# Optimization experiments

Measured on AMD Instinct MI355X. Metric: run time of the kernel, lower is better.

## Reference

```python
import jax, jax.numpy as jnp
import numpy as np

B, N, D, H = 4, 2048, 1024, 16
DH = D // H  # 64
EPS = 1e-5


def setup_inputs() -> dict:
    key = jax.random.key(0)
    k1, k2, k3, k4 = jax.random.split(key, 4)
    return {
        "x": jax.random.normal(k1, (B, N, D), dtype=jnp.float32),
        "g_ln": jnp.ones((D,), dtype=jnp.float32),
        "Wq": jax.random.normal(k2, (D, D), dtype=jnp.float32) * 0.02,
        "Wkv": jax.random.normal(k3, (D, 2 * D), dtype=jnp.float32) * 0.02,
        "Wo": jax.random.normal(k4, (D, D), dtype=jnp.float32) * 0.02,
    }


def reference(x, g_ln, Wq, Wkv, Wo):
    # LayerNorm (gamma only, no bias), as in repo-style LayerNorm
    mu = jnp.mean(x, axis=-1, keepdims=True)
    var = jnp.mean(jnp.square(x - mu), axis=-1, keepdims=True)
    xn = (x - mu) * jax.lax.rsqrt(var + EPS) * g_ln

    b, n, d = xn.shape
    q = (xn @ Wq).reshape(b, n, H, DH).transpose(0, 2, 1, 3)  # b h n d
    kv = xn @ Wkv
    k, v = jnp.split(kv, 2, axis=-1)
    k = k.reshape(b, n, H, DH).transpose(0, 2, 1, 3)
    v = v.reshape(b, n, H, DH).transpose(0, 2, 1, 3)

    scale = DH ** -0.5
    dots = jnp.einsum('bhid,bhjd->bhij', q, k) * scale

    # causal mask: mask out j > i
    mask_value = -jnp.finfo(dots.dtype).max
    causal = jnp.triu(jnp.ones((n, n), dtype=bool), k=1)
    dots = jnp.where(causal, mask_value, dots)

    # softmax in float32 (attn_fn = partial(F.softmax, dtype=torch.float32))
    attn = jax.nn.softmax(dots.astype(jnp.float32), axis=-1).astype(dots.dtype)

    out = jnp.einsum('bhij,bhjd->bhid', attn, v)
    out = out.transpose(0, 2, 1, 3).reshape(b, n, d)  # b n (h d)
    return out @ Wo
```

## Files before the change

kernel.cpp:

```cpp
#include <hip/hip_runtime.h>

typedef __bf16 bf16x8 __attribute__((ext_vector_type(8)));
typedef float  f32x4  __attribute__((ext_vector_type(4)));
typedef unsigned short u16;

typedef __attribute__((address_space(3))) unsigned lds_u32;
typedef __attribute__((address_space(1))) unsigned glob_u32;

__device__ __forceinline__ void gll16(const void* g, void* l) {
  __builtin_amdgcn_global_load_lds(
      (const glob_u32*)(unsigned long long)g,
      (lds_u32*)(unsigned)(unsigned long long)l, 16, 0, 0);
}

__device__ __forceinline__ u16 cvt_bf16(float f) {
  union { float f; unsigned u; } c; c.f = f;
  unsigned u = c.u;
  return (u16)((u + 0x7FFFu + ((u >> 16) & 1u)) >> 16);
}

__global__ void __launch_bounds__(256) transpose_cvt(const float* __restrict__ W,
                                                     u16* __restrict__ WT,
                                                     int K, int N) {
  __shared__ float t[32][33];
  int n0 = blockIdx.x * 32, k0 = blockIdx.y * 32;
  int tx = threadIdx.x, ty = threadIdx.y;
#pragma unroll
  for (int i = 0; i < 4; i++)
    t[ty + i * 8][tx] = W[(size_t)(k0 + ty + i * 8) * N + n0 + tx];
  __syncthreads();
#pragma unroll
  for (int i = 0; i < 4; i++)
    WT[(size_t)(n0 + ty + i * 8) * K + k0 + tx] = cvt_bf16(t[tx][ty + i * 8]);
}

__global__ void __launch_bounds__(256) ln_kernel(const float* __restrict__ x,
                                                 const float* __restrict__ g,
                                                 u16* __restrict__ xn) {
  int row = blockIdx.x, tid = threadIdx.x;
  const float4* xr = (const float4*)(x + (size_t)row * 1024);
  float4 v = xr[tid];
  float s  = v.x + v.y + v.z + v.w;
  float ss = v.x * v.x + v.y * v.y + v.z * v.z + v.w * v.w;
#pragma unroll
  for (int off = 32; off > 0; off >>= 1) {
    s  += __shfl_down(s, off);
    ss += __shfl_down(ss, off);
  }
  __shared__ float red[8];
  if ((tid & 63) == 0) { red[(tid >> 6) * 2] = s; red[(tid >> 6) * 2 + 1] = ss; }
  __syncthreads();
  s  = red[0] + red[2] + red[4] + red[6];
  ss = red[1] + red[3] + red[5] + red[7];
  float mean = s * (1.0f / 1024.0f);
  float var  = ss * (1.0f / 1024.0f) - mean * mean;
  float inv  = rsqrtf(var + 1e-5f);
  float4 gv = ((const float4*)g)[tid];
  unsigned p0 = (unsigned)cvt_bf16((v.x - mean) * inv * gv.x) |
                ((unsigned)cvt_bf16((v.y - mean) * inv * gv.y) << 16);
  unsigned p1 = (unsigned)cvt_bf16((v.z - mean) * inv * gv.z) |
                ((unsigned)cvt_bf16((v.w - mean) * inv * gv.w) << 16);
  uint2 o; o.x = p0; o.y = p1;
  *(uint2*)(xn + (size_t)row * 1024 + tid * 4) = o;
}

template <int EPI>
__global__ void __launch_bounds__(256) gemm_bt(const u16* __restrict__ A,
                                               const u16* __restrict__ BT,
                                               u16* __restrict__ oQ, u16* __restrict__ oK,
                                               u16* __restrict__ oVt, float* __restrict__ oF,
                                               int M, int N, int K) {
  __shared__ u16 As[128 * 64];
  __shared__ u16 Bs[128 * 64];
  int tiles_n = N >> 7;
  int tm = blockIdx.x / tiles_n, tn = blockIdx.x % tiles_n;
  int tid = threadIdx.x, w = tid >> 6, l = tid & 63;
  int wr = w >> 1, wc = w & 1;
  f32x4 acc[4][4] = {};
  const u16* Abase = A + (size_t)(tm * 128) * K;
  const u16* Bbase = BT + (size_t)(tn * 128) * K;

  for (int k0 = 0; k0 < K; k0 += 64) {
#pragma unroll
    for (int t = 0; t < 4; t++) {
      int gi  = t * 256 + tid;
      int o   = gi * 16;
      int row = o >> 7;
      int sb  = o ^ ((row & 7) << 4);
      int col = (sb >> 1) & 63;
      gll16(Abase + (size_t)row * K + k0 + col, (char*)As + t * 4096 + w * 1024);
      gll16(Bbase + (size_t)row * K + k0 + col, (char*)Bs + t * 4096 + w * 1024);
    }
    __syncthreads();
#pragma unroll
    for (int ks = 0; ks < 2; ks++) {
      bf16x8 af[4], bfr[4];
      int kb = ks * 64 + ((l >> 4) << 4);
#pragma unroll
      for (int m = 0; m < 4; m++) {
        int row  = wr * 64 + m * 16 + (l & 15);
        int byte = (row * 128 + kb) ^ ((l & 7) << 4);
        af[m] = *(const bf16x8*)((const char*)As + byte);
      }
#pragma unroll
      for (int n = 0; n < 4; n++) {
        int row  = wc * 64 + n * 16 + (l & 15);
        int byte = (row * 128 + kb) ^ ((l & 7) << 4);
        bfr[n] = *(const bf16x8*)((const char*)Bs + byte);
      }
#pragma unroll
      for (int m = 0; m < 4; m++)
#pragma unroll
        for (int n = 0; n < 4; n++)
          acc[m][n] = __builtin_amdgcn_mfma_f32_16x16x32_bf16(af[m], bfr[n], acc[m][n], 0, 0, 0);
    }
    __syncthreads();
  }

#pragma unroll
  for (int m = 0; m < 4; m++)
#pragma unroll
    for (int n = 0; n < 4; n++)
#pragma unroll
      for (int r = 0; r < 4; r++) {
        int rt = tm * 128 + wr * 64 + m * 16 + ((l >> 4) << 2) + r;
        int c  = tn * 128 + wc * 64 + n * 16 + (l & 15);
        float v = acc[m][n][r];
        if constexpr (EPI == 0) {
          int b = rt >> 11, nn = rt & 2047;
          u16 bv = cvt_bf16(v);
          if (c < 1024) {
            int h = c >> 6, dh = c & 63;
            oQ[((((size_t)b * 16 + h) * 2048) + nn) * 64 + dh] = bv;
          } else if (c < 2048) {
            int c2 = c - 1024, h = c2 >> 6, dh = c2 & 63;
            oK[((((size_t)b * 16 + h) * 2048) + nn) * 64 + dh] = bv;
          } else {
            int c2 = c - 2048, h = c2 >> 6, dh = c2 & 63;
            oVt[((((size_t)b * 16 + h) * 64) + dh) * 2048 + nn] = bv;
          }
        } else {
          oF[(size_t)rt * 1024 + c] = v;
        }
      }
}

__global__ void __launch_bounds__(64, 2) attn_kernel(const u16* __restrict__ Q,
                                                     const u16* __restrict__ Kb,
                                                     const u16* __restrict__ Vt,
                                                     u16* __restrict__ Ao) {
  __shared__ u16 P[32 * 64];
  int bx = blockIdx.x;
  int bh = bx >> 5;
  int pair = bx & 31;
  int l = threadIdx.x;
  const u16* Qb    = Q  + (size_t)bh * 2048 * 64;
  const u16* Kbase = Kb + (size_t)bh * 2048 * 64;
  const u16* Vbase = Vt + (size_t)bh * 64 * 2048;
  char* Pw = (char*)P;
  int b = bh >> 4, h = bh & 15;
  const float SCL = 0.125f * 1.44269504f;

#pragma unroll
  for (int seg = 0; seg < 2; seg++) {
    int ws = seg ? (63 - pair) : pair;
    int q0 = ws * 32;
    int nkb = (ws >> 1) + 1;

    bf16x8 aq[2][2];
#pragma unroll
    for (int m = 0; m < 2; m++)
#pragma unroll
      for (int ks = 0; ks < 2; ks++)
        aq[m][ks] = *(const bf16x8*)(Qb + (size_t)(q0 + m * 16 + (l & 15)) * 64 + ks * 32 + ((l >> 4) << 3));

    f32x4 O[2][4] = {};
    float mrun[2][4], lrun[2][4];
#pragma unroll
    for (int m = 0; m < 2; m++)
#pragma unroll
      for (int r = 0; r < 4; r++) { mrun[m][r] = -1e30f; lrun[m][r] = 0.f; }

    bf16x8 bk[4][2], bkn[4][2];
#pragma unroll
    for (int nf = 0; nf < 4; nf++)
#pragma unroll
      for (int ks = 0; ks < 2; ks++)
        bk[nf][ks] = *(const bf16x8*)(Kbase + (size_t)(nf * 16 + (l & 15)) * 64 + ks * 32 + ((l >> 4) << 3));

    for (int kbi = 0; kbi < nkb; kbi++) {
      int k0 = kbi * 64;
      bf16x8 bv[4][2];
#pragma unroll
      for (int nf = 0; nf < 4; nf++)
#pragma unroll
        for (int ks = 0; ks < 2; ks++)
          bv[nf][ks] = *(const bf16x8*)(Vbase + (size_t)(nf * 16 + (l & 15)) * 2048 + k0 + ks * 32 + ((l >> 4) << 3));
      if (kbi + 1 < nkb) {
        int k1 = k0 + 64;
#pragma unroll
        for (int nf = 0; nf < 4; nf++)
#pragma unroll
          for (int ks = 0; ks < 2; ks++)
            bkn[nf][ks] = *(const bf16x8*)(Kbase + (size_t)(k1 + nf * 16 + (l & 15)) * 64 + ks * 32 + ((l >> 4) << 3));
      }

      f32x4 s[2][4] = {};
#pragma unroll
      for (int m = 0; m < 2; m++)
#pragma unroll
        for (int nf = 0; nf < 4; nf++)
#pragma unroll
          for (int ks = 0; ks < 2; ks++)
            s[m][nf] = __builtin_amdgcn_mfma_f32_16x16x32_bf16(aq[m][ks], bk[nf][ks], s[m][nf], 0, 0, 0);

      int colb = k0 + (l & 15);
#pragma unroll
      for (int m = 0; m < 2; m++) {
        int rowb = q0 + m * 16 + ((l >> 4) << 2);
        float scl[4];
#pragma unroll
        for (int nf = 0; nf < 4; nf++) {
          int col = colb + nf * 16;
#pragma unroll
          for (int r = 0; r < 4; r++) {
            float v = s[m][nf][r] * SCL;
            if (col > rowb + r) v = -1e30f;
            s[m][nf][r] = v;
          }
        }
#pragma unroll
        for (int r = 0; r < 4; r++) {
          float mx = fmaxf(fmaxf(s[m][0][r], s[m][1][r]), fmaxf(s[m][2][r], s[m][3][r]));
          mx = fmaxf(mx, __shfl_xor(mx, 1));
          mx = fmaxf(mx, __shfl_xor(mx, 2));
          mx = fmaxf(mx, __shfl_xor(mx, 4));
          mx = fmaxf(mx, __shfl_xor(mx, 8));
          float mn = fmaxf(mrun[m][r], mx);
          float sc = exp2f(mrun[m][r] - mn);
          mrun[m][r] = mn;
          float rs = 0.f;
#pragma unroll
          for (int nf = 0; nf < 4; nf++) {
            float p = exp2f(s[m][nf][r] - mn);
            s[m][nf][r] = p;
            rs += p;
          }
          rs += __shfl_xor(rs, 1);
          rs += __shfl_xor(rs, 2);
          rs += __shfl_xor(rs, 4);
          rs += __shfl_xor(rs, 8);
          lrun[m][r] = lrun[m][r] * sc + rs;
          scl[r] = sc;
        }
#pragma unroll
        for (int nf = 0; nf < 4; nf++)
#pragma unroll
          for (int r = 0; r < 4; r++) O[m][nf][r] *= scl[r];
      }

#pragma unroll
      for (int m = 0; m < 2; m++)
#pragma unroll
        for (int nf = 0; nf < 4; nf++)
#pragma unroll
          for (int r = 0; r < 4; r++) {
            int row  = m * 16 + ((l >> 4) << 2) + r;
            int byte = (row * 128 + ((nf * 16 + (l & 15)) << 1)) ^ ((row & 7) << 4);
            *(u16*)(Pw + byte) = cvt_bf16(s[m][nf][r]);
          }

      bf16x8 pa[2][2];
#pragma unroll
      for (int m = 0; m < 2; m++)
#pragma unroll
        for (int ks = 0; ks < 2; ks++) {
          int row  = m * 16 + (l & 15);
          int byte = (row * 128 + ks * 64 + ((l >> 4) << 4)) ^ ((row & 7) << 4);
          pa[m][ks] = *(const bf16x8*)(Pw + byte);
        }
#pragma unroll
      for (int m = 0; m < 2; m++)
#pragma unroll
        for (int nf = 0; nf < 4; nf++)
#pragma unroll
          for (int ks = 0; ks < 2; ks++)
            O[m][nf] = __builtin_amdgcn_mfma_f32_16x16x32_bf16(pa[m][ks], bv[nf][ks], O[m][nf], 0, 0, 0);

#pragma unroll
      for (int nf = 0; nf < 4; nf++)
#pragma unroll
        for (int ks = 0; ks < 2; ks++) bk[nf][ks] = bkn[nf][ks];
    }

#pragma unroll
    for (int m = 0; m < 2; m++)
#pragma unroll
      for (int r = 0; r < 4; r++) {
        float rinv = 1.0f / lrun[m][r];
#pragma unroll
        for (int nf = 0; nf < 4; nf++) {
          int row = q0 + m * 16 + ((l >> 4) << 2) + r;
          int col = h * 64 + nf * 16 + (l & 15);
          Ao[((size_t)b * 2048 + row) * 1024 + col] = cvt_bf16(O[m][nf][r] * rinv);
        }
      }
  }
}

extern "C" void kernel_launch(void* const* d_in, const int* in_sizes, int n_in,
                              void* d_out, int out_size, void* d_ws, size_t ws_size,
                              hipStream_t stream) {
  const float* x   = (const float*)d_in[0];
  const float* g   = (const float*)d_in[1];
  const float* Wq  = (const float*)d_in[2];
  const float* Wkv = (const float*)d_in[3];
  const float* Wo  = (const float*)d_in[4];
  float* out = (float*)d_out;
  char* ws = (char*)d_ws;

  u16* WT  = (u16*)(ws);
  u16* WoT = (u16*)(ws + 6291456);
  u16* xn  = (u16*)(ws + 8388608);
  u16* Qb  = (u16*)(ws + 25165824);
  u16* Kb  = (u16*)(ws + 41943040);
  u16* Vt  = (u16*)(ws + 58720256);
  u16* Ao  = (u16*)(ws + 75497472);

  transpose_cvt<<<dim3(32, 32), dim3(32, 8), 0, stream>>>(Wq, WT, 1024, 1024);
  transpose_cvt<<<dim3(64, 32), dim3(32, 8), 0, stream>>>(Wkv, WT + 1024 * 1024, 1024, 2048);
  transpose_cvt<<<dim3(32, 32), dim3(32, 8), 0, stream>>>(Wo, WoT, 1024, 1024);
  ln_kernel<<<8192, 256, 0, stream>>>(x, g, xn);
  gemm_bt<0><<<64 * 24, 256, 0, stream>>>(xn, WT, Qb, Kb, Vt, nullptr, 8192, 3072, 1024);
  attn_kernel<<<2048, 64, 0, stream>>>(Qb, Kb, Vt, Ao);
  gemm_bt<1><<<64 * 8, 256, 0, stream>>>(Ao, WoT, nullptr, nullptr, nullptr, out, 8192, 1024, 1024);
}
```

Baseline: 367.1 us.

## Stage GEMM epilogue through LDS, fold softmax scale into Q, lazy rescaling

The QKV GEMM epilogue now writes through a swizzled LDS tile so Q/K/V^T reach global memory as 16-byte vector stores, and it folds the softmax scale (including log2e) into Q. Both kernels remap block indices for L2 locality: the GEMM groups blocks in chunks of 8, and attention interleaves heads. The attention loop masks only the diagonal block, skips the max and rescale step unless some row's max grows by more than 8 (a wave-wide vote), defers the row-sum shuffles to the end, and uses the hardware exp2. The lazy rescale trades some bf16 precision in P, since unnormalised values can reach 2^8, for much less per-iteration shuffle and exp work.

```diff
diff --git a/kernel.cpp b/kernel.cpp
--- a/kernel.cpp
+++ b/kernel.cpp
@@ -18,6 +18,8 @@
   unsigned u = c.u;
   return (u16)((u + 0x7FFFu + ((u >> 16) & 1u)) >> 16);
 }
+
+#define QSCALE 0.18033688011112042f
 
 __global__ void __launch_bounds__(256) transpose_cvt(const float* __restrict__ W,
                                                      u16* __restrict__ WT,
@@ -70,10 +72,14 @@
                                                u16* __restrict__ oQ, u16* __restrict__ oK,
                                                u16* __restrict__ oVt, float* __restrict__ oF,
                                                int M, int N, int K) {
-  __shared__ u16 As[128 * 64];
-  __shared__ u16 Bs[128 * 64];
+  __shared__ u16 smem[128 * 128];
+  u16* As = smem;
+  u16* Bs = smem + 128 * 64;
   int tiles_n = N >> 7;
-  int tm = blockIdx.x / tiles_n, tn = blockIdx.x % tiles_n;
+  int cpx = gridDim.x >> 3;
+  int wg  = (int)blockIdx.x;
+  int swz = (wg & 7) * cpx + (wg >> 3);
+  int tm = swz / tiles_n, tn = swz % tiles_n;
   int tid = threadIdx.x, w = tid >> 6, l = tid & 63;
   int wr = w >> 1, wc = w & 1;
   f32x4 acc[4][4] = {};
@@ -117,32 +123,59 @@
     __syncthreads();
   }
 
-#pragma unroll
-  for (int m = 0; m < 4; m++)
-#pragma unroll
-    for (int n = 0; n < 4; n++)
-#pragma unroll
-      for (int r = 0; r < 4; r++) {
-        int rt = tm * 128 + wr * 64 + m * 16 + ((l >> 4) << 2) + r;
-        int c  = tn * 128 + wc * 64 + n * 16 + (l & 15);
-        float v = acc[m][n][r];
-        if constexpr (EPI == 0) {
-          int b = rt >> 11, nn = rt & 2047;
-          u16 bv = cvt_bf16(v);
-          if (c < 1024) {
-            int h = c >> 6, dh = c & 63;
-            oQ[((((size_t)b * 16 + h) * 2048) + nn) * 64 + dh] = bv;
-          } else if (c < 2048) {
-            int c2 = c - 1024, h = c2 >> 6, dh = c2 & 63;
-            oK[((((size_t)b * 16 + h) * 2048) + nn) * 64 + dh] = bv;
-          } else {
-            int c2 = c - 2048, h = c2 >> 6, dh = c2 & 63;
-            oVt[((((size_t)b * 16 + h) * 64) + dh) * 2048 + nn] = bv;
-          }
+  if constexpr (EPI == 0) {
+    int c_base = tn * 128;
+    bool isV = (c_base >= 2048);
+    float qs = (c_base < 1024) ? QSCALE : 1.0f;
+#pragma unroll
+    for (int m = 0; m < 4; m++)
+#pragma unroll
+      for (int n = 0; n < 4; n++)
+#pragma unroll
+        for (int r = 0; r < 4; r++) {
+          int rt2 = wr * 64 + m * 16 + ((l >> 4) << 2) + r;
+          int c2  = wc * 64 + n * 16 + (l & 15);
+          u16 bv16 = cvt_bf16(acc[m][n][r] * qs);
+          int byte = isV ? ((c2 * 256 + rt2 * 2) ^ ((c2 & 7) << 4))
+                         : ((rt2 * 256 + c2 * 2) ^ ((rt2 & 7) << 4));
+          *(u16*)((char*)smem + byte) = bv16;
+        }
+    __syncthreads();
+    int b = (tm * 128) >> 11;
+    int nbase = (tm * 128) & 2047;
+#pragma unroll
+    for (int i = 0; i < 8; i++) {
+      int ch = i * 256 + tid;
+      int row = ch >> 4, off = ch & 15;
+      uint4 d = *(const uint4*)((const char*)smem + ((row * 256 + off * 16) ^ ((row & 7) << 4)));
+      if (isV) {
+        int dh = row & 63;
+        int h  = ((c_base - 2048) >> 6) + (row >> 6);
+        *(uint4*)(oVt + ((((size_t)b * 16 + h) * 64) + dh) * 2048 + nbase + off * 8) = d;
+      } else {
+        int cg = c_base + off * 8;
+        int nn = nbase + row;
+        if (cg < 1024) {
+          int h = cg >> 6, dh0 = cg & 63;
+          *(uint4*)(oQ + ((((size_t)b * 16 + h) * 2048) + nn) * 64 + dh0) = d;
         } else {
-          oF[(size_t)rt * 1024 + c] = v;
-        }
-      }
+          int c2g = cg - 1024, h = c2g >> 6, dh0 = c2g & 63;
+          *(uint4*)(oK + ((((size_t)b * 16 + h) * 2048) + nn) * 64 + dh0) = d;
+        }
+      }
+    }
+  } else {
+#pragma unroll
+    for (int m = 0; m < 4; m++)
+#pragma unroll
+      for (int n = 0; n < 4; n++)
+#pragma unroll
+        for (int r = 0; r < 4; r++) {
+          int rt = tm * 128 + wr * 64 + m * 16 + ((l >> 4) << 2) + r;
+          int c  = tn * 128 + wc * 64 + n * 16 + (l & 15);
+          oF[(size_t)rt * 1024 + c] = acc[m][n][r];
+        }
+  }
 }
 
 __global__ void __launch_bounds__(64, 2) attn_kernel(const u16* __restrict__ Q,
@@ -151,15 +184,14 @@
                                                      u16* __restrict__ Ao) {
   __shared__ u16 P[32 * 64];
   int bx = blockIdx.x;
-  int bh = bx >> 5;
-  int pair = bx & 31;
+  int bh = ((bx & 7) << 3) | (bx >> 8);
+  int pair = (bx >> 3) & 31;
   int l = threadIdx.x;
   const u16* Qb    = Q  + (size_t)bh * 2048 * 64;
   const u16* Kbase = Kb + (size_t)bh * 2048 * 64;
   const u16* Vbase = Vt + (size_t)bh * 64 * 2048;
   char* Pw = (char*)P;
   int b = bh >> 4, h = bh & 15;
-  const float SCL = 0.125f * 1.44269504f;
 
 #pragma unroll
   for (int seg = 0; seg < 2; seg++) {
@@ -175,11 +207,11 @@
         aq[m][ks] = *(const bf16x8*)(Qb + (size_t)(q0 + m * 16 + (l & 15)) * 64 + ks * 32 + ((l >> 4) << 3));
 
     f32x4 O[2][4] = {};
-    float mrun[2][4], lrun[2][4];
+    float mrun[2][4], lpart[2][4];
 #pragma unroll
     for (int m = 0; m < 2; m++)
 #pragma unroll
-      for (int r = 0; r < 4; r++) { mrun[m][r] = -1e30f; lrun[m][r] = 0.f; }
+      for (int r = 0; r < 4; r++) { mrun[m][r] = -1e30f; lpart[m][r] = 0.f; }
 
     bf16x8 bk[4][2], bkn[4][2];
 #pragma unroll
@@ -214,61 +246,64 @@
           for (int ks = 0; ks < 2; ks++)
             s[m][nf] = __builtin_amdgcn_mfma_f32_16x16x32_bf16(aq[m][ks], bk[nf][ks], s[m][nf], 0, 0, 0);
 
-      int colb = k0 + (l & 15);
-#pragma unroll
-      for (int m = 0; m < 2; m++) {
-        int rowb = q0 + m * 16 + ((l >> 4) << 2);
-        float scl[4];
-#pragma unroll
-        for (int nf = 0; nf < 4; nf++) {
-          int col = colb + nf * 16;
+      if (kbi == nkb - 1) {
+        int colb = k0 + (l & 15);
+#pragma unroll
+        for (int m = 0; m < 2; m++) {
+          int rowb = q0 + m * 16 + ((l >> 4) << 2);
+#pragma unroll
+          for (int nf = 0; nf < 4; nf++) {
+            int col = colb + nf * 16;
+#pragma unroll
+            for (int r = 0; r < 4; r++)
+              if (col > rowb + r) s[m][nf][r] = -1e30f;
+          }
+        }
+      }
+
+      float lmx[2][4];
+      bool need = false;
+#pragma unroll
+      for (int m = 0; m < 2; m++)
+#pragma unroll
+        for (int r = 0; r < 4; r++) {
+          lmx[m][r] = fmaxf(fmaxf(s[m][0][r], s[m][1][r]), fmaxf(s[m][2][r], s[m][3][r]));
+          need |= (lmx[m][r] > mrun[m][r] + 8.0f);
+        }
+      if (__any(need)) {
+#pragma unroll
+        for (int m = 0; m < 2; m++)
 #pragma unroll
           for (int r = 0; r < 4; r++) {
-            float v = s[m][nf][r] * SCL;
-            if (col > rowb + r) v = -1e30f;
-            s[m][nf][r] = v;
+            float mx = lmx[m][r];
+            mx = fmaxf(mx, __shfl_xor(mx, 1));
+            mx = fmaxf(mx, __shfl_xor(mx, 2));
+            mx = fmaxf(mx, __shfl_xor(mx, 4));
+            mx = fmaxf(mx, __shfl_xor(mx, 8));
+            float mn = fmaxf(mrun[m][r], mx);
+            float sc = __builtin_amdgcn_exp2f(mrun[m][r] - mn);
+            mrun[m][r] = mn;
+            lpart[m][r] *= sc;
+#pragma unroll
+            for (int nf = 0; nf < 4; nf++) O[m][nf][r] *= sc;
           }
-        }
+      }
+
+#pragma unroll
+      for (int m = 0; m < 2; m++)
 #pragma unroll
         for (int r = 0; r < 4; r++) {
-          float mx = fmaxf(fmaxf(s[m][0][r], s[m][1][r]), fmaxf(s[m][2][r], s[m][3][r]));
-          mx = fmaxf(mx, __shfl_xor(mx, 1));
-          mx = fmaxf(mx, __shfl_xor(mx, 2));
-          mx = fmaxf(mx, __shfl_xor(mx, 4));
-          mx = fmaxf(mx, __shfl_xor(mx, 8));
-          float mn = fmaxf(mrun[m][r], mx);
-          float sc = exp2f(mrun[m][r] - mn);
-          mrun[m][r] = mn;
-          float rs = 0.f;
+          int rowl = m * 16 + ((l >> 4) << 2) + r;
+          float ps = 0.f;
 #pragma unroll
           for (int nf = 0; nf < 4; nf++) {
-            float p = exp2f(s[m][nf][r] - mn);
-            s[m][nf][r] = p;
-            rs += p;
+            float p = __builtin_amdgcn_exp2f(s[m][nf][r] - mrun[m][r]);
+            ps += p;
+            int byte = (rowl * 128 + ((nf * 16 + (l & 15)) << 1)) ^ ((rowl & 7) << 4);
+            *(u16*)(Pw + byte) = cvt_bf16(p);
           }
-          rs += __shfl_xor(rs, 1);
-          rs += __shfl_xor(rs, 2);
-          rs += __shfl_xor(rs, 4);
-          rs += __shfl_xor(rs, 8);
-          lrun[m][r] = lrun[m][r] * sc + rs;
-          scl[r] = sc;
-        }
-#pragma unroll
-        for (int nf = 0; nf < 4; nf++)
-#pragma unroll
-          for (int r = 0; r < 4; r++) O[m][nf][r] *= scl[r];
-      }
-
-#pragma unroll
-      for (int m = 0; m < 2; m++)
-#pragma unroll
-        for (int nf = 0; nf < 4; nf++)
-#pragma unroll
-          for (int r = 0; r < 4; r++) {
-            int row  = m * 16 + ((l >> 4) << 2) + r;
-            int byte = (row * 128 + ((nf * 16 + (l & 15)) << 1)) ^ ((row & 7) << 4);
-            *(u16*)(Pw + byte) = cvt_bf16(s[m][nf][r]);
-          }
+          lpart[m][r] += ps;
+        }
 
       bf16x8 pa[2][2];
 #pragma unroll
@@ -297,10 +332,15 @@
     for (int m = 0; m < 2; m++)
 #pragma unroll
       for (int r = 0; r < 4; r++) {
-        float rinv = 1.0f / lrun[m][r];
+        float ls = lpart[m][r];
+        ls += __shfl_xor(ls, 1);
+        ls += __shfl_xor(ls, 2);
+        ls += __shfl_xor(ls, 4);
+        ls += __shfl_xor(ls, 8);
+        float rinv = 1.0f / ls;
+        int row = q0 + m * 16 + ((l >> 4) << 2) + r;
 #pragma unroll
         for (int nf = 0; nf < 4; nf++) {
-          int row = q0 + m * 16 + ((l >> 4) << 2) + r;
           int col = h * 64 + nf * 16 + (l & 15);
           Ao[((size_t)b * 2048 + row) * 1024 + col] = cvt_bf16(O[m][nf][r] * rinv);
         }
```

Measured after the change: 318.5 us. 1.15x faster.
